# Performance work log

Hardware: AMD Instinct MI355X
Metric: run time of the kernel (lower is better)

## Reference

```python
import jax, jax.numpy as jnp
import numpy as np

N_NODES = 80000
N_EDGES = 1280000
D_IN = 64
D_OUT = 64


def setup_inputs() -> dict:
    key = jax.random.key(0)
    k1, k2, k3, k4 = jax.random.split(key, 4)
    x = jax.random.normal(k1, (N_NODES, D_IN), dtype=jnp.float32)
    edge_index = jax.random.randint(k2, (2, N_EDGES), 0, N_NODES, dtype=jnp.int64)
    # GCNConv linear weight (stored as [in, out] for x @ W) and post-aggregation bias
    W = jax.random.normal(k3, (D_IN, D_OUT), dtype=jnp.float32) / jnp.sqrt(jnp.float32(D_IN))
    b = jax.random.normal(k4, (D_OUT,), dtype=jnp.float32) * 0.01
    return {"x": x, "edge_index": edge_index, "W": W, "b": b}


def reference(x, edge_index, W, b):
    # GCNConv (PyG defaults): add self-loops, symmetric normalization,
    # linear transform, scatter-add aggregation, bias; then ReLU.
    N = x.shape[0]
    loops = jnp.arange(N, dtype=edge_index.dtype)
    src = jnp.concatenate([edge_index[0], loops])  # [E+N]
    dst = jnp.concatenate([edge_index[1], loops])  # [E+N]

    # degree over destination nodes (self-loops included -> deg >= 1)
    deg = jax.ops.segment_sum(jnp.ones_like(src, dtype=x.dtype), dst, num_segments=N)
    dinv = jax.lax.rsqrt(jnp.where(deg > 0, deg, jnp.ones_like(deg)))
    norm = dinv[src] * dinv[dst]  # [E+N]

    h = x @ W  # [N, D_OUT]
    msg = h[src] * norm[:, None]  # gather + scale, [E+N, D_OUT]
    agg = jax.ops.segment_sum(msg, dst, num_segments=N)  # scatter-add, [N, D_OUT]
    return jax.nn.relu(agg + b)
```

## Files before the change

### kernel.cpp

```cpp
#include <hip/hip_runtime.h>
#include <hip/hip_bf16.h>

#define D 64
#define NODES_PER_BIN 256
#define BIN_SHIFT 8
#define CAP 5120
#define TILE 2048
#define EPT 8
#define WSTR 72

typedef short bf16x8 __attribute__((ext_vector_type(8)));
typedef float f32x4 __attribute__((ext_vector_type(4)));
typedef unsigned short u16x8 __attribute__((ext_vector_type(8)));

__device__ __forceinline__ float bf2f(unsigned short u) {
    union { unsigned int i; float f; } c; c.i = (unsigned int)u << 16; return c.f;
}
__device__ __forceinline__ unsigned short f2bf(float f) {
    union { float f; unsigned int i; } c; c.f = f;
    unsigned int x = c.i;
    return (unsigned short)((x + 0x7fffu + ((x >> 16) & 1u)) >> 16);
}

__global__ void k_zero_i(int* __restrict__ p, int n) {
    int i = threadIdx.x;
    if (i < n) p[i] = 0;
}

__global__ __launch_bounds__(256) void k_passA(const int* __restrict__ src,
                                               const int* __restrict__ dst,
                                               int* __restrict__ cursor,
                                               int* __restrict__ binned,
                                               int E, int NBINS) {
    __shared__ int hist[512];
    __shared__ int reservedBase[512];
    int tid = threadIdx.x;
    long long t0 = (long long)blockIdx.x * TILE;
    int cnt_tile = (int)((E - t0 < TILE) ? (E - t0) : TILE);

    for (int i = tid; i < 512; i += 256) hist[i] = 0;
    __syncthreads();

    int val[EPT]; int bn[EPT]; int rk[EPT];
#pragma unroll
    for (int k = 0; k < EPT; ++k) {
        int i = k * 256 + tid;
        if (i < cnt_tile) {
            int e = (int)t0 + i;
            int s = src[e], d = dst[e];
            bn[k] = d >> BIN_SHIFT;
            val[k] = s | ((d & (NODES_PER_BIN - 1)) << 17);
            rk[k] = atomicAdd(&hist[bn[k]], 1);
        } else { bn[k] = -1; val[k] = 0; rk[k] = 0; }
    }
    __syncthreads();
    for (int i = tid; i < NBINS; i += 256)
        reservedBase[i] = (hist[i] > 0) ? atomicAdd(&cursor[i], hist[i]) : 0;
    __syncthreads();
#pragma unroll
    for (int k = 0; k < EPT; ++k)
        if (bn[k] >= 0)
            binned[bn[k] * CAP + reservedBase[bn[k]] + rk[k]] = val[k];
}

__global__ __launch_bounds__(256) void k_passB(const int* __restrict__ binned,
                                               const int* __restrict__ binCount,
                                               int* __restrict__ sorted_src,
                                               int* __restrict__ row_ptr,
                                               int* __restrict__ counts,
                                               float* __restrict__ dinv, int N) {
    __shared__ int eLDS[CAP];
    __shared__ int srt[CAP];
    __shared__ int cnt[NODES_PER_BIN];
    __shared__ int nodeOff[NODES_PER_BIN];
    __shared__ int sA[NODES_PER_BIN], sB[NODES_PER_BIN];
    int tid = threadIdx.x;
    int b = blockIdx.x;
    int lo = b << BIN_SHIFT;
    int nNodes = N - lo; if (nNodes > NODES_PER_BIN) nNodes = NODES_PER_BIN;
    int base = b * CAP;
    int size = binCount[b]; if (size > CAP) size = CAP;

    for (int i = tid; i < size; i += 256) eLDS[i] = binned[base + i];
    cnt[tid] = 0;
    __syncthreads();
    for (int i = tid; i < size; i += 256) atomicAdd(&cnt[eLDS[i] >> 17], 1);
    __syncthreads();
    sA[tid] = cnt[tid];
    __syncthreads();
    int *a = sA, *bb = sB;
    for (int dd = 1; dd < 256; dd <<= 1) {
        bb[tid] = a[tid] + (tid >= dd ? a[tid - dd] : 0);
        __syncthreads();
        int* t = a; a = bb; bb = t;
    }
    nodeOff[tid] = (tid > 0) ? a[tid - 1] : 0;
    __syncthreads();
    if (tid < nNodes) {
        int c = cnt[tid];
        row_ptr[lo + tid] = base + nodeOff[tid];
        counts[lo + tid] = c;
        dinv[lo + tid] = rsqrtf(1.0f + (float)c);
    }
    __syncthreads();
    cnt[tid] = 0;
    __syncthreads();
    for (int i = tid; i < size; i += 256) {
        int v = eLDS[i];
        int dl = v >> 17;
        int r = atomicAdd(&cnt[dl], 1);
        srt[nodeOff[dl] + r] = v & 0x1FFFF;
    }
    __syncthreads();
    for (int i = tid; i < size; i += 256) sorted_src[base + i] = srt[i];
}

__global__ __launch_bounds__(256) void k_gemm_v4(const float* __restrict__ x,
                                                 const float* __restrict__ W,
                                                 const float* __restrict__ dinv,
                                                 unsigned short* __restrict__ g, int N) {
    __shared__ unsigned short WtHi[D * WSTR];
    __shared__ unsigned short WtLo[D * WSTR];
    int tid = threadIdx.x;
    for (int idx = tid; idx < D * D; idx += 256) {
        int k = idx >> 6, j = idx & 63;
        float w = W[idx];
        unsigned short hi = f2bf(w);
        WtHi[j * WSTR + k] = hi;
        WtLo[j * WSTR + k] = f2bf(w - bf2f(hi));
    }
    __syncthreads();

    int lane = tid & 63;
    int wid  = tid >> 6;
    int lcol = lane & 15;
    int lkg  = lane >> 4;

    bf16x8 Bhi[2][4], Blo[2][4];
#pragma unroll
    for (int s = 0; s < 2; ++s)
#pragma unroll
        for (int n = 0; n < 4; ++n) {
            int j = n * 16 + lcol;
            int k = s * 32 + lkg * 8;
            Bhi[s][n] = *(const bf16x8*)&WtHi[j * WSTR + k];
            Blo[s][n] = *(const bf16x8*)&WtLo[j * WSTR + k];
        }

    const int nTiles = (N + 15) >> 4;
    const int stride = gridDim.x * 4;
    for (int t = blockIdx.x * 4 + wid; t < nTiles; t += stride) {
        int r0 = t * 16;
        int arow = r0 + lcol;
        bool rok = (arow < N);
        bf16x8 Ahi[2], Alo[2];
#pragma unroll
        for (int s = 0; s < 2; ++s) {
            float4 v0{0.f,0.f,0.f,0.f}, v1{0.f,0.f,0.f,0.f};
            if (rok) {
                const float4* p = (const float4*)&x[(size_t)arow * D + s * 32 + lkg * 8];
                v0 = p[0]; v1 = p[1];
            }
            float xv[8] = {v0.x, v0.y, v0.z, v0.w, v1.x, v1.y, v1.z, v1.w};
#pragma unroll
            for (int e = 0; e < 8; ++e) {
                unsigned short hi = f2bf(xv[e]);
                Ahi[s][e] = (short)hi;
                Alo[s][e] = (short)f2bf(xv[e] - bf2f(hi));
            }
        }

        f32x4 acc[4];
#pragma unroll
        for (int n = 0; n < 4; ++n) {
            f32x4 c = {0.f, 0.f, 0.f, 0.f};
            c = __builtin_amdgcn_mfma_f32_16x16x32_bf16(Ahi[0], Bhi[0][n], c, 0, 0, 0);
            c = __builtin_amdgcn_mfma_f32_16x16x32_bf16(Ahi[1], Bhi[1][n], c, 0, 0, 0);
            c = __builtin_amdgcn_mfma_f32_16x16x32_bf16(Alo[0], Bhi[0][n], c, 0, 0, 0);
            c = __builtin_amdgcn_mfma_f32_16x16x32_bf16(Alo[1], Bhi[1][n], c, 0, 0, 0);
            c = __builtin_amdgcn_mfma_f32_16x16x32_bf16(Ahi[0], Blo[0][n], c, 0, 0, 0);
            c = __builtin_amdgcn_mfma_f32_16x16x32_bf16(Ahi[1], Blo[1][n], c, 0, 0, 0);
            acc[n] = c;
        }

#pragma unroll
        for (int i = 0; i < 4; ++i) {
            int orow = r0 + lkg * 4 + i;
            if (orow < N) {
                float dv = dinv[orow];
#pragma unroll
                for (int n = 0; n < 4; ++n)
                    g[(size_t)orow * D + n * 16 + lcol] = f2bf(acc[n][i] * dv);
            }
        }
    }
}

__global__ __launch_bounds__(256) void k_aggregate7(const int* __restrict__ row_ptr,
                                                    const int* __restrict__ counts,
                                                    const int* __restrict__ sorted_src,
                                                    const u16x8* __restrict__ g8,
                                                    const float* __restrict__ dinv,
                                                    const float* __restrict__ b,
                                                    float* __restrict__ out, int N) {
    int n = (blockIdx.x * 256 + threadIdx.x) >> 6;
    int lane = threadIdx.x & 63;
    if (n >= N) return;
    int q8 = lane >> 3;
    int p8 = lane & 7;
    int start = row_ptr[n];
    int cnt = counts[n];
    const int* sp = sorted_src + start;

    float a0 = 0.f, a1 = 0.f, a2 = 0.f, a3 = 0.f;
    float a4 = 0.f, a5 = 0.f, a6 = 0.f, a7 = 0.f;
    if (q8 == 0) {
        u16x8 v = g8[(size_t)n * 8 + p8];
        a0 = bf2f(v[0]); a1 = bf2f(v[1]); a2 = bf2f(v[2]); a3 = bf2f(v[3]);
        a4 = bf2f(v[4]); a5 = bf2f(v[5]); a6 = bf2f(v[6]); a7 = bf2f(v[7]);
    }

#define LIDX8(jg, I, M)                                        \
    {                                                          \
        int e_ = (jg) * 8 + q8;                                \
        bool ok_ = (e_ < cnt);                                 \
        I = ok_ ? sp[e_] : n;                                  \
        M = ok_ ? 1.f : 0.f;                                   \
    }
#define CONS8(V, M)                                            \
    {                                                          \
        a0 = fmaf(M, bf2f(V[0]), a0);                          \
        a1 = fmaf(M, bf2f(V[1]), a1);                          \
        a2 = fmaf(M, bf2f(V[2]), a2);                          \
        a3 = fmaf(M, bf2f(V[3]), a3);                          \
        a4 = fmaf(M, bf2f(V[4]), a4);                          \
        a5 = fmaf(M, bf2f(V[5]), a5);                          \
        a6 = fmaf(M, bf2f(V[6]), a6);                          \
        a7 = fmaf(M, bf2f(V[7]), a7);                          \
    }

    int i0, i1, i2, i3;
    float m0, m1, m2, m3;
    LIDX8(0, i0, m0); LIDX8(1, i1, m1); LIDX8(2, i2, m2); LIDX8(3, i3, m3);
    u16x8 u0 = g8[(size_t)i0 * 8 + p8];
    u16x8 u1 = g8[(size_t)i1 * 8 + p8];
    u16x8 u2 = g8[(size_t)i2 * 8 + p8];
    u16x8 u3 = g8[(size_t)i3 * 8 + p8];
    CONS8(u0, m0); CONS8(u1, m1); CONS8(u2, m2); CONS8(u3, m3);

    int ng = (cnt + 7) >> 3;
    for (int jg = 4; jg < ng; ++jg) {
        int I; float M;
        LIDX8(jg, I, M);
        u16x8 U = g8[(size_t)I * 8 + p8];
        CONS8(U, M);
    }
#undef LIDX8
#undef CONS8

#define FOLD(A) A += __shfl_xor(A, 8, 64); A += __shfl_xor(A, 16, 64); A += __shfl_xor(A, 32, 64);
    FOLD(a0) FOLD(a1) FOLD(a2) FOLD(a3) FOLD(a4) FOLD(a5) FOLD(a6) FOLD(a7)
#undef FOLD

    if (q8 == 0) {
        float dv = dinv[n];
        const float4* b4 = (const float4*)b;
        float4 bl = b4[p8 * 2 + 0];
        float4 bh = b4[p8 * 2 + 1];
        float4 r0, r1;
        r0.x = fmaxf(fmaf(a0, dv, bl.x), 0.f);
        r0.y = fmaxf(fmaf(a1, dv, bl.y), 0.f);
        r0.z = fmaxf(fmaf(a2, dv, bl.z), 0.f);
        r0.w = fmaxf(fmaf(a3, dv, bl.w), 0.f);
        r1.x = fmaxf(fmaf(a4, dv, bh.x), 0.f);
        r1.y = fmaxf(fmaf(a5, dv, bh.y), 0.f);
        r1.z = fmaxf(fmaf(a6, dv, bh.z), 0.f);
        r1.w = fmaxf(fmaf(a7, dv, bh.w), 0.f);
        float4* o4 = (float4*)out;
        o4[(size_t)n * 16 + p8 * 2 + 0] = r0;
        o4[(size_t)n * 16 + p8 * 2 + 1] = r1;
    }
}


__global__ void k_deg_init(float* __restrict__ deg, int N) {
    int i = blockIdx.x * blockDim.x + threadIdx.x;
    if (i < N) deg[i] = 1.0f;
}
__global__ void k_deg_count(const int* __restrict__ dst, float* __restrict__ deg, int E) {
    int i = blockIdx.x * blockDim.x + threadIdx.x;
    if (i < E) atomicAdd(&deg[dst[i]], 1.0f);
}
__global__ void k_dinv_f(float* __restrict__ deg, int N) {
    int i = blockIdx.x * blockDim.x + threadIdx.x;
    if (i < N) deg[i] = rsqrtf(deg[i]);
}
__global__ __launch_bounds__(256) void k_gemm_fb(const float* __restrict__ x, const float* __restrict__ W,
                                                 const float* __restrict__ dinv, float* __restrict__ g,
                                                 float* __restrict__ acc, int N) {
    __shared__ float Ws[D * D];
    __shared__ float xs[4][D];
    int tid = threadIdx.x;
    for (int t = tid; t < D * D; t += 256) Ws[t] = W[t];
    int rg = tid >> 6, j = tid & 63;
    int r = blockIdx.x * 4 + rg;
    if (r < N) xs[rg][j] = x[r * D + j];
    __syncthreads();
    if (r < N) {
        float s = 0.f;
#pragma unroll
        for (int k = 0; k < D; ++k) s = fmaf(xs[rg][k], Ws[k * D + j], s);
        s *= dinv[r];
        g[r * D + j] = s;
        acc[r * D + j] = s;
    }
}
__global__ __launch_bounds__(256) void k_scatter_fb(const int* __restrict__ src, const int* __restrict__ dst,
                                                    const float* __restrict__ g, float* __restrict__ acc, int E) {
    long long idx = (long long)blockIdx.x * blockDim.x + threadIdx.x;
    int e = (int)(idx >> 6), j = (int)(idx & 63);
    if (e < E) atomicAdd(&acc[dst[e] * D + j], g[src[e] * D + j]);
}
__global__ void k_final_fb(float* __restrict__ out, const float* __restrict__ dinv,
                           const float* __restrict__ b, int N) {
    int idx = blockIdx.x * blockDim.x + threadIdx.x;
    if (idx < N * D) {
        int r = idx >> 6, j = idx & 63;
        float v = out[idx] * dinv[r] + b[j];
        out[idx] = v > 0.f ? v : 0.f;
    }
}


extern "C" void kernel_launch(void* const* d_in, const int* in_sizes, int n_in,
                              void* d_out, int out_size, void* d_ws, size_t ws_size,
                              hipStream_t stream) {
    const float* x  = (const float*)d_in[0];
    const int*   ei = (const int*)d_in[1];
    const float* W  = (const float*)d_in[2];
    const float* b  = (const float*)d_in[3];
    float* out = (float*)d_out;

    const int N = in_sizes[0] / D;
    const int E = in_sizes[1] / 2;
    const int* src = ei;
    const int* dst = ei + E;
    const int NBINS = (N + NODES_PER_BIN - 1) >> BIN_SHIFT;

    size_t off = 0;
    auto take = [&](size_t bytes) { size_t p = off; off = (off + bytes + 255) & ~(size_t)255; return p; };
    char* base = (char*)d_ws;
    size_t o_counts  = take((size_t)N * 4);
    size_t o_dinv    = take((size_t)N * 4);
    size_t o_rowptr  = take((size_t)N * 4);
    size_t o_cursor  = take(512 * 4);
    size_t o_sorted  = take((size_t)NBINS * CAP * 4);
    size_t o_binned  = take((size_t)NBINS * CAP * 4);
    size_t o_g       = take((size_t)N * D * 2);
    size_t req1 = off;

    bool tier1_ok = (ws_size >= req1) && (N <= (1 << 17)) && (NBINS <= 512);

    if (tier1_ok) {
        int* counts     = (int*)(base + o_counts);
        float* dinv     = (float*)(base + o_dinv);
        int* row_ptr    = (int*)(base + o_rowptr);
        int* cursor     = (int*)(base + o_cursor);
        int* sorted_src = (int*)(base + o_sorted);
        int* binned     = (int*)(base + o_binned);
        unsigned short* g = (unsigned short*)(base + o_g);

        k_zero_i<<<1, 512, 0, stream>>>(cursor, NBINS);
        k_passA<<<(E + TILE - 1) / TILE, 256, 0, stream>>>(src, dst, cursor, binned, E, NBINS);
        k_passB<<<NBINS, 256, 0, stream>>>(binned, cursor, sorted_src, row_ptr, counts, dinv, N);
        k_gemm_v4<<<625, 256, 0, stream>>>(x, W, dinv, g, N);
        long long thr = (long long)N * 64;
        k_aggregate7<<<(int)((thr + 255) / 256), 256, 0, stream>>>(row_ptr, counts, sorted_src,
                                                                   (const u16x8*)g, dinv, b, out, N);
        return;
    }

    {
        float* deg = (float*)d_ws;
        float* g   = (float*)((char*)d_ws + (size_t)N * sizeof(float));
        k_deg_init<<<(N + 255) / 256, 256, 0, stream>>>(deg, N);
        k_deg_count<<<(E + 255) / 256, 256, 0, stream>>>(dst, deg, E);
        k_dinv_f<<<(N + 255) / 256, 256, 0, stream>>>(deg, N);
        k_gemm_fb<<<(N + 3) / 4, 256, 0, stream>>>(x, W, deg, g, out, N);
        long long total = (long long)E * D;
        k_scatter_fb<<<(int)((total + 255) / 256), 256, 0, stream>>>(src, dst, g, out, E);
        k_final_fb<<<(N * D + 255) / 256, 256, 0, stream>>>(out, deg, b, N);
    }
}
```

Before: 85.09 us.

## Split each node's aggregation across two wavefronts with LDS reduction

The aggregation kernel now gives each destination node two wavefronts instead of one. The two waves take alternating groups of 8 edges, and their partial sums are combined through shared memory after a block barrier. This doubles the number of waves per node, aiming for more memory-level parallelism on the gather. The cost is a __syncthreads, LDS traffic, twice the index and count loads, and many half-idle waves, since the average degree is about 16 so each wave handles only about one group.

```diff
diff --git a/kernel.cpp b/kernel.cpp
--- a/kernel.cpp
+++ b/kernel.cpp
@@ -196,25 +196,30 @@
     }
 }
 
-__global__ __launch_bounds__(256) void k_aggregate7(const int* __restrict__ row_ptr,
+__global__ __launch_bounds__(256) void k_aggregate8(const int* __restrict__ row_ptr,
                                                     const int* __restrict__ counts,
                                                     const int* __restrict__ sorted_src,
                                                     const u16x8* __restrict__ g8,
                                                     const float* __restrict__ dinv,
                                                     const float* __restrict__ b,
                                                     float* __restrict__ out, int N) {
-    int n = (blockIdx.x * 256 + threadIdx.x) >> 6;
-    int lane = threadIdx.x & 63;
-    if (n >= N) return;
+    __shared__ float part[4][8][8];
+    int tid = threadIdx.x;
+    int w = tid >> 6;
+    int lane = tid & 63;
+    int n = blockIdx.x * 2 + (w >> 1);
+    int h = w & 1;
     int q8 = lane >> 3;
     int p8 = lane & 7;
-    int start = row_ptr[n];
-    int cnt = counts[n];
+    bool nok = (n < N);
+    int start = 0, cnt = 0;
+    if (nok) { start = row_ptr[n]; cnt = counts[n]; }
     const int* sp = sorted_src + start;
+    int safe = nok ? n : 0;
 
     float a0 = 0.f, a1 = 0.f, a2 = 0.f, a3 = 0.f;
     float a4 = 0.f, a5 = 0.f, a6 = 0.f, a7 = 0.f;
-    if (q8 == 0) {
+    if (nok && h == 0 && q8 == 0) {
         u16x8 v = g8[(size_t)n * 8 + p8];
         a0 = bf2f(v[0]); a1 = bf2f(v[1]); a2 = bf2f(v[2]); a3 = bf2f(v[3]);
         a4 = bf2f(v[4]); a5 = bf2f(v[5]); a6 = bf2f(v[6]); a7 = bf2f(v[7]);
@@ -224,7 +229,7 @@
     {                                                          \
         int e_ = (jg) * 8 + q8;                                \
         bool ok_ = (e_ < cnt);                                 \
-        I = ok_ ? sp[e_] : n;                                  \
+        I = ok_ ? sp[e_] : safe;                               \
         M = ok_ ? 1.f : 0.f;                                   \
     }
 #define CONS8(V, M)                                            \
@@ -239,17 +244,14 @@
         a7 = fmaf(M, bf2f(V[7]), a7);                          \
     }
 
-    int i0, i1, i2, i3;
-    float m0, m1, m2, m3;
-    LIDX8(0, i0, m0); LIDX8(1, i1, m1); LIDX8(2, i2, m2); LIDX8(3, i3, m3);
+    int i0, i1; float m0, m1;
+    LIDX8(h, i0, m0); LIDX8(h + 2, i1, m1);
     u16x8 u0 = g8[(size_t)i0 * 8 + p8];
     u16x8 u1 = g8[(size_t)i1 * 8 + p8];
-    u16x8 u2 = g8[(size_t)i2 * 8 + p8];
-    u16x8 u3 = g8[(size_t)i3 * 8 + p8];
-    CONS8(u0, m0); CONS8(u1, m1); CONS8(u2, m2); CONS8(u3, m3);
+    CONS8(u0, m0); CONS8(u1, m1);
 
     int ng = (cnt + 7) >> 3;
-    for (int jg = 4; jg < ng; ++jg) {
+    for (int jg = 4 + h; jg < ng; jg += 2) {
         int I; float M;
         LIDX8(jg, I, M);
         u16x8 U = g8[(size_t)I * 8 + p8];
@@ -263,6 +265,15 @@
 #undef FOLD
 
     if (q8 == 0) {
+        part[w][p8][0] = a0; part[w][p8][1] = a1; part[w][p8][2] = a2; part[w][p8][3] = a3;
+        part[w][p8][4] = a4; part[w][p8][5] = a5; part[w][p8][6] = a6; part[w][p8][7] = a7;
+    }
+    __syncthreads();
+    if (nok && h == 0 && q8 == 0) {
+        a0 += part[w + 1][p8][0]; a1 += part[w + 1][p8][1];
+        a2 += part[w + 1][p8][2]; a3 += part[w + 1][p8][3];
+        a4 += part[w + 1][p8][4]; a5 += part[w + 1][p8][5];
+        a6 += part[w + 1][p8][6]; a7 += part[w + 1][p8][7];
         float dv = dinv[n];
         const float4* b4 = (const float4*)b;
         float4 bl = b4[p8 * 2 + 0];
@@ -374,9 +385,8 @@
         k_passA<<<(E + TILE - 1) / TILE, 256, 0, stream>>>(src, dst, cursor, binned, E, NBINS);
         k_passB<<<NBINS, 256, 0, stream>>>(binned, cursor, sorted_src, row_ptr, counts, dinv, N);
         k_gemm_v4<<<625, 256, 0, stream>>>(x, W, dinv, g, N);
-        long long thr = (long long)N * 64;
-        k_aggregate7<<<(int)((thr + 255) / 256), 256, 0, stream>>>(row_ptr, counts, sorted_src,
-                                                                   (const u16x8*)g, dinv, b, out, N);
+        k_aggregate8<<<(N + 1) / 2, 256, 0, stream>>>(row_ptr, counts, sorted_src,
+                                                      (const u16x8*)g, dinv, b, out, N);
         return;
     }
 
```

New measurement: 106.3 us. 25.0% more time.
